# Kernel tuning notes

Measured on AMD Instinct MI355X. Metric: run time of the kernel, lower is better.

## Reference

```python
import jax, jax.numpy as jnp
import numpy as np

STRIDE = 16
BASE_SIZE = 16
RATIOS = (0.5, 1.0, 2.0)
SCALES = (8, 16, 32)
N_PRE_NMS = 3000
N_POST_NMS = 300
NMS_THRESH = 0.5
MIN_SIZE = 16.0


def _make_anchors(H, W):
    # base anchors centered at 0, [x1,y1,x2,y2]; ratio-major, scale-minor
    ba = []
    for r in RATIOS:
        for s in SCALES:
            w = BASE_SIZE * s * np.sqrt(1.0 / r)
            h = BASE_SIZE * s * np.sqrt(r)
            ba.append([-0.5 * w, -0.5 * h, 0.5 * w, 0.5 * h])
    ba = np.asarray(ba, np.float32)  # (9,4)
    xs = np.arange(W, dtype=np.float32) * STRIDE
    ys = np.arange(H, dtype=np.float32) * STRIDE
    X, Y = np.meshgrid(xs, ys)  # (H,W), h-major matches NHWC flatten order
    shifts = np.stack([X.ravel(), Y.ravel(), X.ravel(), Y.ravel()], 1)  # (H*W,4)
    return jnp.asarray((shifts[:, None, :] + ba[None, :, :]).reshape(-1, 4))


def _conv(x, w, b, pad):
    y = jax.lax.conv_general_dilated(x, w, (1, 1), [(pad, pad), (pad, pad)],
                                     dimension_numbers=('NCHW', 'OIHW', 'NCHW'))
    return y + b[None, :, None, None]


def _nms_keep(boxes, valid, thresh):
    # greedy NMS on score-sorted boxes; classic +1 area convention
    x1, y1, x2, y2 = boxes[:, 0], boxes[:, 1], boxes[:, 2], boxes[:, 3]
    areas = (x2 - x1 + 1.0) * (y2 - y1 + 1.0)
    n = boxes.shape[0]
    idx = jnp.arange(n)

    def body(i, keep):
        xx1 = jnp.maximum(x1[i], x1)
        yy1 = jnp.maximum(y1[i], y1)
        xx2 = jnp.minimum(x2[i], x2)
        yy2 = jnp.minimum(y2[i], y2)
        inter = jnp.clip(xx2 - xx1 + 1.0, 0.0) * jnp.clip(yy2 - yy1 + 1.0, 0.0)
        iou = inter / (areas[i] + areas - inter)
        sup = jnp.any((idx < i) & keep & (iou > thresh))
        return keep.at[i].set(keep[i] & (~sup))

    return jax.lax.fori_loop(0, n, body, valid)


def _rpn_forward(x, w_base, b_base, w_cls, b_cls, w_reg, b_reg):
    B, _, H, W = x.shape  # B == 1
    base = jax.nn.relu(_conv(x, w_base, b_base, 1))           # (1,512,H,W)
    locs = _conv(base, w_reg, b_reg, 0).transpose(0, 2, 3, 1).reshape(-1, 4)  # (H*W*9,4)
    cls = _conv(base, w_cls, b_cls, 0).transpose(0, 2, 3, 1).reshape(1, -1, 2)
    fg = jax.nn.softmax(cls, axis=-1)[0, :, 1]                # (H*W*9,)

    anchors = _make_anchors(H, W)
    aw = anchors[:, 2] - anchors[:, 0]
    ah = anchors[:, 3] - anchors[:, 1]
    acx = anchors[:, 0] + 0.5 * aw
    acy = anchors[:, 1] + 0.5 * ah
    cx = locs[:, 0] * aw + acx
    cy = locs[:, 1] * ah + acy
    w = jnp.exp(locs[:, 2]) * aw
    h = jnp.exp(locs[:, 3]) * ah
    boxes = jnp.stack([cx - 0.5 * w, cy - 0.5 * h, cx + 0.5 * w, cy + 0.5 * h], 1)

    img_w = float(W * STRIDE)
    img_h = float(H * STRIDE)
    boxes = jnp.stack([jnp.clip(boxes[:, 0], 0.0, img_w),
                       jnp.clip(boxes[:, 1], 0.0, img_h),
                       jnp.clip(boxes[:, 2], 0.0, img_w),
                       jnp.clip(boxes[:, 3], 0.0, img_h)], 1)
    valid = ((boxes[:, 2] - boxes[:, 0]) >= MIN_SIZE) & ((boxes[:, 3] - boxes[:, 1]) >= MIN_SIZE)

    masked = jnp.where(valid, fg, -jnp.inf)
    top_scores, top_idx = jax.lax.top_k(masked, N_PRE_NMS)   # descending, == argsort top-k
    bsel = boxes[top_idx]
    vsel = valid[top_idx]

    keep = _nms_keep(bsel, vsel, NMS_THRESH)
    rank = jnp.cumsum(keep.astype(jnp.int32)) - 1
    pos = jnp.where(keep & (rank < N_POST_NMS), rank, N_POST_NMS)  # out-of-range -> dropped
    rois = jnp.zeros((N_POST_NMS, 4), bsel.dtype).at[pos].set(bsel, mode='drop')
    # original scores[:n_post] over dim0 of shape (1,n_pre) is a no-op -> full (1,3000)
    return rois, top_scores[None, :]


def setup_inputs() -> dict:
    key = jax.random.key(0)
    ks = jax.random.split(key, 7)
    H = W = 128
    return {
        'x': jax.random.normal(ks[0], (1, 1024, H, W), jnp.float32),
        'w_base': jax.random.normal(ks[1], (512, 1024, 3, 3), jnp.float32) * 0.01,
        'b_base': jax.random.normal(ks[2], (512,), jnp.float32) * 0.01,
        'w_cls': jax.random.normal(ks[3], (18, 512, 1, 1), jnp.float32) * 0.01,
        'b_cls': jax.random.normal(ks[4], (18,), jnp.float32) * 0.01,
        'w_reg': jax.random.normal(ks[5], (36, 512, 1, 1), jnp.float32) * 0.01,
        'b_reg': jax.random.normal(ks[6], (36,), jnp.float32) * 0.01,
    }


def reference(x, w_base, b_base, w_cls, b_cls, w_reg, b_reg):
    return _rpn_forward(x, w_base, b_base, w_cls, b_cls, w_reg, b_reg)
```

## Files before the change

### kernel.cpp

```cpp
#include <hip/hip_runtime.h>
#include <cmath>

typedef unsigned long long u64;
typedef __attribute__((ext_vector_type(8))) short short8;
typedef __attribute__((ext_vector_type(4))) float f32x4;
typedef __attribute__((ext_vector_type(4))) double f64x4;

#define N_ANCH   147456
#define N_SCREEN 3600
#define N_PRE    3000
#define N_POST   300
#define NWORDS   47
#define SEL_CAP  4096

__device__ inline short f2bf(float f) {
    unsigned u = __float_as_uint(f);
    unsigned r = u + 0x7FFFu + ((u >> 16) & 1u);
    return (short)(r >> 16);
}

__global__ __launch_bounds__(256) void rpn_prep_xT(const float* __restrict__ x,
                                                   short* __restrict__ xT) {
    __shared__ short tile[32][258];
    const int h  = blockIdx.x;
    const int w0 = blockIdx.y * 32;
    const int c0 = blockIdx.z * 256;
    const int tid = threadIdx.x;
    const int wi = tid & 31, cs = tid >> 5;
    #pragma unroll
    for (int it = 0; it < 32; ++it) {
        int c = it * 8 + cs;
        float v = x[(size_t)(c0 + c) * 16384 + h * 128 + w0 + wi];
        tile[wi][c] = f2bf(v);
    }
    __syncthreads();
    #pragma unroll
    for (int it = 0; it < 32; ++it) {
        int i = tid + it * 256;
        int wj = i >> 8, c = i & 255;
        xT[((size_t)h * 128 + w0 + wj) * 1024 + c0 + c] = tile[wj][c];
    }
}

__global__ __launch_bounds__(256) void rpn_prep_wbf(const float* __restrict__ wb,
                                                    short* __restrict__ wT) {
    __shared__ float wtile[2304];
    const int oc = blockIdx.x;
    const int c0 = blockIdx.y * 256;
    const int tid = threadIdx.x;
    #pragma unroll
    for (int it = 0; it < 9; ++it) {
        int i = tid + it * 256;
        wtile[i] = wb[(size_t)oc * 9216 + c0 * 9 + i];
    }
    __syncthreads();
    #pragma unroll
    for (int it = 0; it < 9; ++it) {
        int i = tid + it * 256;
        int t = i >> 8, c = i & 255;
        wT[((size_t)t * 512 + oc) * 1024 + c0 + c] = f2bf(wtile[c * 9 + t]);
    }
}

__global__ __launch_bounds__(256) void rpn_prep_w(const float* __restrict__ wb,
                                                  float* __restrict__ wt) {
    __shared__ float tile[64][65];
    const int bx = blockIdx.x;
    const int by = blockIdx.y;
    const int tid = threadIdx.x;
    #pragma unroll
    for (int it = 0; it < 16; ++it) {
        int i = tid + it * 256;
        int r = i >> 6, c = i & 63;
        tile[r][c] = wb[(size_t)(by * 64 + r) * 9216 + bx * 64 + c];
    }
    __syncthreads();
    #pragma unroll
    for (int it = 0; it < 16; ++it) {
        int i = tid + it * 256;
        int r = i >> 6, c = i & 63;
        wt[(size_t)(bx * 64 + r) * 512 + by * 64 + c] = tile[c][r];
    }
}

__global__ void rpn_prep_wht(const float* __restrict__ wc, const float* __restrict__ wr,
                             float* __restrict__ wht) {
    int i = blockIdx.x * 256 + threadIdx.x;
    if (i >= 512 * 56) return;
    int c = i / 56, k = i - c * 56;
    float v = 0.f;
    if (k < 18)       v = wc[k * 512 + c];
    else if (k < 54)  v = wr[(k - 18) * 512 + c];
    wht[i] = v;
}

#define STAGE_LOADM(WREG, XREG, CN)                                            \
    {                                                                          \
        _Pragma("unroll")                                                      \
        for (int it = 0; it < 9; ++it)                                         \
            WREG[it] = *(const short8*)&wT[wgo[it] + (CN)];                    \
        _Pragma("unroll")                                                      \
        for (int it = 0; it < 4; ++it)                                         \
            XREG[it] = (xgo[it] >= 0) ? *(const short8*)&xT[xgo[it] + (CN)]    \
                                      : zer;                                   \
    }
#define STAGE_WRITEM(WREG, XREG)                                               \
    {                                                                          \
        _Pragma("unroll")                                                      \
        for (int it = 0; it < 9; ++it) *(short8*)&wsm[wlo[it]] = WREG[it];     \
        _Pragma("unroll")                                                      \
        for (int it = 0; it < 4; ++it)                                         \
            if (xlo[it] >= 0) *(short8*)&xsm[xlo[it]] = XREG[it];              \
    }
#define MFMA_CHUNKM()                                                          \
    {                                                                          \
        _Pragma("unroll")                                                      \
        for (int t = 0; t < 9; ++t) {                                          \
            int kh = t / 3, kw = t - kh * 3;                                   \
            int ra0 = t * 128 + wocB + l15;                                    \
            int ra1 = ra0 + 16;                                                \
            short8 a0 = *(const short8*)&wsm[ra0 * 32 + ((lg ^ ((ra0 >> 1) & 3)) << 3)]; \
            short8 a1 = *(const short8*)&wsm[ra1 * 32 + ((lg ^ ((ra1 >> 1) & 3)) << 3)]; \
            _Pragma("unroll")                                                  \
            for (int nf = 0; nf < 4; ++nf) {                                   \
                int rb = kh * 130 + wpx + nf * 16 + l15 + kw;                  \
                short8 b = *(const short8*)&xsm[rb * 32 + ((lg ^ ((rb >> 1) & 3)) << 3)]; \
                acc[0][nf] = __builtin_amdgcn_mfma_f32_16x16x32_bf16(a0, b, acc[0][nf], 0, 0, 0); \
                acc[1][nf] = __builtin_amdgcn_mfma_f32_16x16x32_bf16(a1, b, acc[1][nf], 0, 0, 0); \
            }                                                                  \
        }                                                                      \
    }

__global__ __launch_bounds__(512, 2) void rpn_screen_mfma(
    const short* __restrict__ xT, const short* __restrict__ wT,
    const float* __restrict__ bb, const float* __restrict__ wht_,
    float* __restrict__ logits) {
    const int row = blockIdx.x;
    const int ocB = blockIdx.y * 128;
    const int tid = threadIdx.x;
    const int wave = tid >> 6, lane = tid & 63;
    const int l15 = lane & 15, lg = lane >> 4;
    const int wocB = (wave & 3) * 32;
    const int wpx  = (wave >> 2) * 64;
    __shared__ __attribute__((aligned(16))) short wsm[1152 * 32];
    __shared__ __attribute__((aligned(16))) short xsm[390 * 32];

    size_t wgo[9];  int wlo[9];
    #pragma unroll
    for (int it = 0; it < 9; ++it) {
        int i = tid + it * 512;
        int r = i >> 2, s = i & 3;
        int t = r >> 7, ocl = r & 127;
        wgo[it] = ((size_t)t * 512 + ocB + ocl) * 1024 + s * 8;
        wlo[it] = r * 32 + ((s ^ ((r >> 1) & 3)) << 3);
    }
    long xgo[4]; int xlo[4];
    #pragma unroll
    for (int it = 0; it < 4; ++it) {
        int i = tid + it * 512;
        xlo[it] = -1; xgo[it] = -1;
        if (i < 1560) {
            int r = i >> 2, s = i & 3;
            int r3 = r / 130, col = r - r3 * 130;
            int h = row - 1 + r3, wc = col - 1;
            xlo[it] = r * 32 + ((s ^ ((r >> 1) & 3)) << 3);
            xgo[it] = (h >= 0 && h < 128 && wc >= 0 && wc < 128)
                      ? (long)(((size_t)h * 128 + wc) * 1024 + s * 8) : -1;
        }
    }

    f32x4 acc[2][4];
    #pragma unroll
    for (int mi = 0; mi < 2; ++mi)
        #pragma unroll
        for (int nf = 0; nf < 4; ++nf)
            acc[mi][nf] = (f32x4){0.f, 0.f, 0.f, 0.f};

    short8 wregA[9], xregA[4], wregB[9], xregB[4];
    const short8 zer = {0, 0, 0, 0, 0, 0, 0, 0};

    STAGE_LOADM(wregA, xregA, 0);
    STAGE_LOADM(wregB, xregB, 32);

    for (int i2 = 0; i2 < 16; ++i2) {
        int cA = i2 * 64;
        __syncthreads();
        STAGE_WRITEM(wregA, xregA);
        __syncthreads();
        if (cA + 64 < 1024) STAGE_LOADM(wregA, xregA, cA + 64);
        MFMA_CHUNKM();
        __syncthreads();
        STAGE_WRITEM(wregB, xregB);
        __syncthreads();
        if (cA + 96 < 1024) STAGE_LOADM(wregB, xregB, cA + 96);
        MFMA_CHUNKM();
    }

    float r_[8][4];
    #pragma unroll
    for (int mi = 0; mi < 2; ++mi)
        #pragma unroll
        for (int rr = 0; rr < 4; ++rr) {
            int ocg = ocB + wocB + mi * 16 + lg * 4 + rr;
            float bv = bb[ocg];
            #pragma unroll
            for (int nf = 0; nf < 4; ++nf)
                r_[mi * 4 + rr][nf] = fmaxf(acc[mi][nf][rr] + bv, 0.f);
        }
    float* lred = (float*)wsm;
    const int pxc = tid >> 2, qqc = tid & 3;
    for (int qc = 0; qc < 14; ++qc) {
        float wq[8][4];
        #pragma unroll
        for (int p = 0; p < 8; ++p) {
            int ocg = ocB + wocB + (p >> 2) * 16 + lg * 4 + (p & 3);
            float4 wv = *(const float4*)&wht_[(size_t)ocg * 56 + qc * 4];
            wq[p][0] = wv.x; wq[p][1] = wv.y; wq[p][2] = wv.z; wq[p][3] = wv.w;
        }
        __syncthreads();
        #pragma unroll
        for (int nf = 0; nf < 4; ++nf) {
            #pragma unroll
            for (int qq = 0; qq < 4; ++qq) {
                float s = 0.f;
                #pragma unroll
                for (int p = 0; p < 8; ++p) s = fmaf(r_[p][nf], wq[p][qq], s);
                s += __shfl_xor(s, 16);
                s += __shfl_xor(s, 32);
                if (lg == 0)
                    lred[(((wave & 3) * 128) + wpx + nf * 16 + l15) * 4 + qq] = s;
            }
        }
        __syncthreads();
        float v = lred[(0 * 128 + pxc) * 4 + qqc] + lred[(1 * 128 + pxc) * 4 + qqc]
                + lred[(2 * 128 + pxc) * 4 + qqc] + lred[(3 * 128 + pxc) * 4 + qqc];
        atomicAdd(&logits[(size_t)(row * 128 + pxc) * 56 + qc * 4 + qqc], v);
    }
}

__global__ void rpn_screen_decode(
    const float* __restrict__ logits, const float* __restrict__ bc,
    const float* __restrict__ br, unsigned* __restrict__ keys32,
    unsigned* __restrict__ hist1) {
    int aidx = blockIdx.x * 256 + threadIdx.x;
    if (aidx >= N_ANCH) return;
    int px = aidx / 9, a = aidx - px * 9;
    int wix = px & 127, hix = px >> 7;
    float Xf = (float)(wix * 16), Yf = (float)(hix * 16);
    int ri = a / 3, si = a - ri * 3;
    double rr  = (ri == 0) ? 0.5 : ((ri == 1) ? 1.0 : 2.0);
    double scl = (si == 0) ? 8.0 : ((si == 1) ? 16.0 : 32.0);
    double wA = 16.0 * scl * sqrt(1.0 / rr);
    double hA = 16.0 * scl * sqrt(rr);
    float c0 = (float)(-0.5 * wA), c1 = (float)(-0.5 * hA);
    float c2 = (float)( 0.5 * wA), c3 = (float)( 0.5 * hA);
    float ax1 = Xf + c0, ay1 = Yf + c1, ax2 = Xf + c2, ay2 = Yf + c3;
    float aw = ax2 - ax1, ah = ay2 - ay1;
    float acx = ax1 + 0.5f * aw, acy = ay1 + 0.5f * ah;
    const float* L = &logits[(size_t)px * 56];
    float l0 = L[2 * a]     + bc[2 * a];
    float l1 = L[2 * a + 1] + bc[2 * a + 1];
    float dx = L[18 + 4 * a + 0] + br[4 * a + 0];
    float dy = L[18 + 4 * a + 1] + br[4 * a + 1];
    float dw = L[18 + 4 * a + 2] + br[4 * a + 2];
    float dh = L[18 + 4 * a + 3] + br[4 * a + 3];
    float cx = dx * aw + acx, cy = dy * ah + acy;
    float bw = expf(dw) * aw, bh = expf(dh) * ah;
    float x1 = fminf(fmaxf(cx - 0.5f * bw, 0.f), 2048.f);
    float y1 = fminf(fmaxf(cy - 0.5f * bh, 0.f), 2048.f);
    float x2 = fminf(fmaxf(cx + 0.5f * bw, 0.f), 2048.f);
    float y2 = fminf(fmaxf(cy + 0.5f * bh, 0.f), 2048.f);
    bool valid = (x2 - x1 >= 12.0f) && (y2 - y1 >= 12.0f);
    float m = fmaxf(l0, l1);
    float e0 = expf(l0 - m), e1 = expf(l1 - m);
    float fg = e1 / (e0 + e1);
    float msk = valid ? fg : -INFINITY;
    unsigned kb = __float_as_uint(msk);
    kb = (kb & 0x80000000u) ? ~kb : (kb | 0x80000000u);
    keys32[aidx] = kb;
    atomicAdd(&hist1[kb >> 16], 1u);
}

__global__ void rpn_select1(const unsigned* __restrict__ hist, unsigned* __restrict__ meta) {
    __shared__ unsigned seg[256];
    __shared__ unsigned suf[257];
    int t = threadIdx.x;
    unsigned s = 0;
    for (int j = 0; j < 256; ++j) s += hist[t * 256 + j];
    seg[t] = s;
    __syncthreads();
    if (t == 0) {
        unsigned run = 0; suf[256] = 0;
        for (int q = 255; q >= 0; --q) { run += seg[q]; suf[q] = run; }
    }
    __syncthreads();
    if (suf[t + 1] < N_SCREEN && suf[t] >= N_SCREEN) {
        unsigned cum = suf[t + 1];
        for (int b = t * 256 + 255; b >= t * 256; --b) {
            unsigned prev = cum;
            cum += hist[b];
            if (cum >= N_SCREEN) { meta[0] = (unsigned)b; meta[1] = prev; break; }
        }
    }
}

__global__ void rpn_hist2(const unsigned* __restrict__ keys, const unsigned* __restrict__ meta,
                          unsigned* __restrict__ hist2) {
    int i = blockIdx.x * 256 + threadIdx.x;
    if (i >= N_ANCH) return;
    unsigned B = meta[0];
    unsigned k = keys[i];
    if ((k >> 16) == B) atomicAdd(&hist2[k & 0xFFFFu], 1u);
}

__global__ void rpn_select2(const unsigned* __restrict__ hist2, unsigned* __restrict__ meta) {
    __shared__ unsigned seg[256];
    __shared__ unsigned suf[257];
    int t = threadIdx.x;
    unsigned s = 0;
    for (int j = 0; j < 256; ++j) s += hist2[t * 256 + j];
    seg[t] = s;
    __syncthreads();
    if (t == 0) {
        unsigned run = 0; suf[256] = 0;
        for (int q = 255; q >= 0; --q) { run += seg[q]; suf[q] = run; }
    }
    __syncthreads();
    unsigned need = N_SCREEN - meta[1];
    if (suf[t + 1] < need && suf[t] >= need) {
        unsigned cum = suf[t + 1];
        for (int b = t * 256 + 255; b >= t * 256; --b) {
            cum += hist2[b];
            if (cum >= need) { meta[3] = (meta[0] << 16) | (unsigned)b; break; }
        }
    }
}

__global__ void rpn_compact(const unsigned* __restrict__ keys, unsigned* meta,
                            int* __restrict__ sel_idx, unsigned* __restrict__ pxflag) {
    int i = blockIdx.x * 256 + threadIdx.x;
    if (i >= N_ANCH) return;
    if (keys[i] >= meta[3]) {
        unsigned pos = atomicAdd(&meta[4], 1u);
        if (pos < SEL_CAP) {
            sel_idx[pos] = i;
            pxflag[i / 9] = 1u;
        }
    }
}

__global__ void rpn_px_compact(const unsigned* __restrict__ pxflag, unsigned* meta,
                               int* __restrict__ pxlist, int* __restrict__ pxslot) {
    int px = blockIdx.x * 256 + threadIdx.x;
    if (px >= 16384) return;
    if (pxflag[px]) {
        int slot = (int)atomicAdd(&meta[5], 1u);
        pxlist[slot] = px;
        pxslot[px] = slot;
    }
}

__global__ __launch_bounds__(256) void rpn_rescue_gemm(
    const float* __restrict__ x, const float* __restrict__ wt,
    const int* __restrict__ pxlist, const unsigned* __restrict__ meta,
    double* __restrict__ base64) {
    int npx = (int)meta[5];
    int s0 = blockIdx.x * 16;
    if (s0 >= npx) return;
    const int tid  = threadIdx.x;
    const int wave = tid >> 6, lane = tid & 63;
    const int l15 = lane & 15, lg = lane >> 4;
    const int ocg = blockIdx.y * 64 + wave * 16;
    __shared__ double xs[144][17];

    f64x4 p1 = (f64x4){0.0, 0.0, 0.0, 0.0};
    f64x4 p2 = (f64x4){0.0, 0.0, 0.0, 0.0};
    p1 = __builtin_amdgcn_mfma_f64_16x16x4f64((double)l15, 1.0, p1, 0, 0, 0);
    p2 = __builtin_amdgcn_mfma_f64_16x16x4f64(1.0, (double)l15, p2, 0, 0, 0);
    int srow[4], scol[4];
    #pragma unroll
    for (int r = 0; r < 4; ++r) {
        srow[r] = (int)(p1[r] * 0.25 + 0.5);
        scol[r] = (int)(p2[r] * 0.25 + 0.5);
    }

    int sp_off[9];
    int ch_of[9];
    #pragma unroll
    for (int it = 0; it < 9; ++it) {
        int j = tid + it * 256;
        int kk = j >> 4, slot = j & 15;
        int cl = kk / 9, tap = kk - cl * 9;
        int sg = s0 + slot;
        int pv = pxlist[(sg < npx) ? sg : s0];
        int yy = (pv >> 7) + tap / 3 - 1;
        int xx = (pv & 127) + tap % 3 - 1;
        sp_off[it] = (yy >= 0 && yy < 128 && xx >= 0 && xx < 128) ? (yy * 128 + xx) : -1;
        ch_of[it] = cl;
    }

    f64x4 acc = (f64x4){0.0, 0.0, 0.0, 0.0};
    float xreg[9];

    #pragma unroll
    for (int it = 0; it < 9; ++it)
        xreg[it] = (sp_off[it] >= 0) ? x[(size_t)ch_of[it] * 16384 + sp_off[it]] : 0.f;

    const size_t wlane = (size_t)(ocg + l15) + (size_t)lg * 512;
    for (int c0 = 0; c0 < 1024; c0 += 16) {
        __syncthreads();
        #pragma unroll
        for (int it = 0; it < 9; ++it) {
            int j = tid + it * 256;
            xs[j >> 4][j & 15] = (double)xreg[it];
        }
        __syncthreads();
        if (c0 + 16 < 1024) {
            #pragma unroll
            for (int it = 0; it < 9; ++it)
                xreg[it] = (sp_off[it] >= 0)
                           ? x[(size_t)(c0 + 16 + ch_of[it]) * 16384 + sp_off[it]] : 0.f;
        }
        const size_t wbase = (size_t)c0 * 4608 + wlane;
        #pragma unroll
        for (int ks = 0; ks < 36; ++ks) {
            double a = xs[ks * 4 + lg][l15];
            double b = (double)wt[wbase + (size_t)ks * 2048];
            acc = __builtin_amdgcn_mfma_f64_16x16x4f64(a, b, acc, 0, 0, 0);
        }
    }
    #pragma unroll
    for (int r = 0; r < 4; ++r) {
        int slot = s0 + srow[r];
        if (slot < npx)
            base64[(size_t)slot * 512 + ocg + scol[r]] = acc[r];
    }
}

__global__ __launch_bounds__(256) void rpn_rescue_heads(
    const double* __restrict__ base64, const float* __restrict__ wht,
    const float* __restrict__ bb, const float* __restrict__ bc,
    const float* __restrict__ br, const unsigned* __restrict__ meta,
    double* __restrict__ logits64) {
    int npx = (int)meta[5]; if (npx > SEL_CAP) npx = SEL_CAP;
    int slot0 = blockIdx.x * 4;
    if (slot0 >= npx) return;
    const int tid = threadIdx.x;
    __shared__ double bs[4][514];
    for (int i = tid; i < 4 * 512; i += 256) {
        int s = i >> 9, c = i & 511;
        int slt = slot0 + s;
        double v = (slt < npx) ? base64[(size_t)slt * 512 + c] : 0.0;
        double r = v + (double)bb[c];
        bs[s][c] = (r > 0.0) ? r : 0.0;
    }
    __syncthreads();
    if (tid < 224) {
        int s = tid / 56, q = tid - s * 56;
        int slt = slot0 + s;
        if (slt < npx) {
            double acc = (q < 18) ? (double)bc[q] : ((q < 54) ? (double)br[q - 18] : 0.0);
            const double* b = bs[s];
            #pragma unroll 8
            for (int c = 0; c < 512; ++c)
                acc = fma(b[c], (double)wht[c * 56 + q], acc);
            logits64[(size_t)slt * 56 + q] = acc;
        }
    }
}

__global__ void rpn_rescue_decode(
    const double* __restrict__ logits64, const int* __restrict__ sel_idx,
    const int* __restrict__ pxslot, const unsigned* __restrict__ meta,
    double* __restrict__ boxes_d, float* __restrict__ sc32, u64* __restrict__ sel) {
    int i = blockIdx.x * 256 + threadIdx.x;
    unsigned M = meta[4]; if (M > SEL_CAP) M = SEL_CAP;
    if (i >= (int)M) return;
    int aidx = sel_idx[i];
    int px = aidx / 9, a = aidx - px * 9;
    int slot = pxslot[px];
    int wix = px & 127, hix = px >> 7;
    float Xf = (float)(wix * 16), Yf = (float)(hix * 16);
    int ri = a / 3, si = a - ri * 3;
    double rr  = (ri == 0) ? 0.5 : ((ri == 1) ? 1.0 : 2.0);
    double scl = (si == 0) ? 8.0 : ((si == 1) ? 16.0 : 32.0);
    double wA = 16.0 * scl * sqrt(1.0 / rr);
    double hA = 16.0 * scl * sqrt(rr);
    float c0 = (float)(-0.5 * wA), c1 = (float)(-0.5 * hA);
    float c2 = (float)( 0.5 * wA), c3 = (float)( 0.5 * hA);
    float ax1 = Xf + c0, ay1 = Yf + c1, ax2 = Xf + c2, ay2 = Yf + c3;
    float awf = ax2 - ax1, ahf = ay2 - ay1;
    float acxf = ax1 + 0.5f * awf, acyf = ay1 + 0.5f * ahf;
    double aw = (double)awf, ah = (double)ahf;
    double acx = (double)acxf, acy = (double)acyf;
    const double* L = &logits64[(size_t)slot * 56];
    double l0 = L[2 * a], l1 = L[2 * a + 1];
    double dx = L[18 + 4 * a + 0], dy = L[18 + 4 * a + 1];
    double dw = L[18 + 4 * a + 2], dh = L[18 + 4 * a + 3];
    double cx = dx * aw + acx, cy = dy * ah + acy;
    double bw = exp(dw) * aw, bh = exp(dh) * ah;
    double x1 = fmin(fmax(cx - 0.5 * bw, 0.0), 2048.0);
    double y1 = fmin(fmax(cy - 0.5 * bh, 0.0), 2048.0);
    double x2 = fmin(fmax(cx + 0.5 * bw, 0.0), 2048.0);
    double y2 = fmin(fmax(cy + 0.5 * bh, 0.0), 2048.0);
    bool valid = (x2 - x1 >= 16.0) && (y2 - y1 >= 16.0);
    double m = fmax(l0, l1);
    double e0 = exp(l0 - m), e1 = exp(l1 - m);
    double fg = e1 / (e0 + e1);
    double msk = valid ? fg : -INFINITY;
    double* bd = &boxes_d[(size_t)aidx * 4];
    bd[0] = x1; bd[1] = y1; bd[2] = x2; bd[3] = y2;
    sc32[aidx] = (float)msk;
    long long ll = __double_as_longlong(msk);
    u64 u = (ll < 0) ? ~(u64)ll : ((u64)ll | 0x8000000000000000ull);
    sel[i] = (u & 0xFFFFFFFFFFFC0000ull) | (u64)(0x3FFFFu - (unsigned)aidx);
}

__global__ __launch_bounds__(1024) void rpn_sort(
    const u64* __restrict__ sel, const unsigned* __restrict__ meta,
    const double* __restrict__ boxes_d, const float* __restrict__ sc32,
    float* __restrict__ out, double* __restrict__ bsel, unsigned* __restrict__ vsel) {
    __shared__ u64 ss[SEL_CAP];
    int tid = threadIdx.x;
    int M = (int)meta[4]; if (M > SEL_CAP) M = SEL_CAP;
    for (int i = tid; i < SEL_CAP; i += 1024) ss[i] = (i < M) ? sel[i] : 0ULL;
    __syncthreads();
    for (int k = 2; k <= SEL_CAP; k <<= 1) {
        for (int j = k >> 1; j > 0; j >>= 1) {
            for (int i = tid; i < SEL_CAP; i += 1024) {
                int l = i ^ j;
                if (l > i) {
                    u64 a = ss[i], b = ss[l];
                    bool desc = (i & k) == 0;
                    if ((a < b) == desc) { ss[i] = b; ss[l] = a; }
                }
            }
            __syncthreads();
        }
    }
    for (int r = tid; r < N_PRE; r += 1024) {
        u64 key = ss[r];
        unsigned idx = 0x3FFFFu - (unsigned)(key & 0x3FFFFull);
        out[N_POST * 4 + r] = sc32[idx];
        const double* bd = &boxes_d[(size_t)idx * 4];
        double* dst = &bsel[(size_t)r * 4];
        dst[0] = bd[0]; dst[1] = bd[1]; dst[2] = bd[2]; dst[3] = bd[3];
        vsel[r] = (key >> 63) ? 1u : 0u;
    }
}

__global__ void rpn_nms_mask(const double* __restrict__ bsel, u64* __restrict__ mask) {
    int t = blockIdx.x * 256 + threadIdx.x;
    if (t >= N_PRE * NWORDS) return;
    int i = t / NWORDS, w = t - i * NWORDS;
    const double* bi = &bsel[(size_t)i * 4];
    double bix1 = bi[0], biy1 = bi[1], bix2 = bi[2], biy2 = bi[3];
    double ai = (bix2 - bix1 + 1.0) * (biy2 - biy1 + 1.0);
    u64 bits = 0ULL;
    int j0 = w * 64;
    for (int jj = 0; jj < 64; ++jj) {
        int j = j0 + jj;
        if (j >= N_PRE || j == i) continue;
        const double* bj = &bsel[(size_t)j * 4];
        double aj = (bj[2] - bj[0] + 1.0) * (bj[3] - bj[1] + 1.0);
        double xx1 = fmax(bix1, bj[0]), yy1 = fmax(biy1, bj[1]);
        double xx2 = fmin(bix2, bj[2]), yy2 = fmin(biy2, bj[3]);
        double iw = fmax(xx2 - xx1 + 1.0, 0.0), ih = fmax(yy2 - yy1 + 1.0, 0.0);
        double inter = iw * ih;
        double iou = inter / (ai + aj - inter);
        if (iou > 0.5) bits |= 1ULL << jj;
    }
    mask[(size_t)i * NWORDS + w] = bits;
}

__global__ __launch_bounds__(64) void rpn_nms_scan(
    const u64* __restrict__ mask, const unsigned* __restrict__ vsel,
    unsigned* __restrict__ keep, unsigned* __restrict__ rank) {
    int lane = threadIdx.x;
    u64 remv = 0ULL;
    int kc = 0;
    u64 pre[8];
    unsigned vpre[8];
    #pragma unroll
    for (int q = 0; q < 8; ++q) {
        pre[q]  = (lane < NWORDS) ? mask[(size_t)q * NWORDS + lane] : 0ULL;
        vpre[q] = vsel[q];
    }
    for (int i0 = 0; i0 < N_PRE; i0 += 8) {
        u64 nxt[8];
        unsigned vnxt[8];
        #pragma unroll
        for (int q = 0; q < 8; ++q) {
            int r = i0 + 8 + q;
            nxt[q]  = (r < N_PRE && lane < NWORDS) ? mask[(size_t)r * NWORDS + lane] : 0ULL;
            vnxt[q] = (r < N_PRE) ? vsel[r] : 0u;
        }
        #pragma unroll
        for (int q = 0; q < 8; ++q) {
            int i = i0 + q;
            int word = i >> 6, bit = i & 63;
            u64 rw = __shfl(remv, word);
            bool sup = (rw >> bit) & 1ULL;
            bool kp = (vpre[q] != 0u) && !sup;
            if (kp) remv |= pre[q];
            if (lane == 0) { keep[i] = kp ? 1u : 0u; rank[i] = (unsigned)kc; }
            kc += kp ? 1 : 0;
        }
        #pragma unroll
        for (int q = 0; q < 8; ++q) { pre[q] = nxt[q]; vpre[q] = vnxt[q]; }
    }
}

__global__ void rpn_finalize(const unsigned* __restrict__ keep, const unsigned* __restrict__ rank,
                             const double* __restrict__ bsel, float* __restrict__ out) {
    int i = blockIdx.x * 256 + threadIdx.x;
    if (i < N_PRE && keep[i] && rank[i] < N_POST) {
        const double* b = &bsel[(size_t)i * 4];
        float4 v = make_float4((float)b[0], (float)b[1], (float)b[2], (float)b[3]);
        ((float4*)out)[rank[i]] = v;
    }
}

extern "C" void kernel_launch(void* const* d_in, const int* in_sizes, int n_in,
                              void* d_out, int out_size, void* d_ws, size_t ws_size,
                              hipStream_t stream) {
    const float* x   = (const float*)d_in[0];
    const float* wb  = (const float*)d_in[1];
    const float* bb  = (const float*)d_in[2];
    const float* wc  = (const float*)d_in[3];
    const float* bc  = (const float*)d_in[4];
    const float* wr  = (const float*)d_in[5];
    const float* br  = (const float*)d_in[6];
    float* out = (float*)d_out;

    char* ws = (char*)d_ws;
    short*    xT       = (short*)(ws);
    float*    wt       = (float*)(ws);
    double*   base64   = (double*)(ws + 18874368);
    short*    wT       = (short*)(ws + 33554432);
    float*    logits32 = (float*)(ws + 42991616);
    float*    wht      = (float*)(ws + 46661632);
    double*   logits64 = (double*)(ws + 46776320);
    double*   boxes_d  = (double*)(ws + 48611328);
    float*    sc32     = (float*)(ws + 53329920);
    unsigned* keys32   = (unsigned*)(ws + 53919744);
    unsigned* hist1    = (unsigned*)(ws + 54509568);
    unsigned* hist2    = (unsigned*)(ws + 54771712);
    unsigned* meta     = (unsigned*)(ws + 55033856);
    int*      sel_idx  = (int*)(ws + 55034112);
    u64*      sel      = (u64*)(ws + 55050496);
    unsigned* pxflag   = (unsigned*)(ws + 55083264);
    int*      pxlist   = (int*)(ws + 55148800);
    int*      pxslot   = (int*)(ws + 55165184);
    double*   bsel     = (double*)(ws + 55230720);
    unsigned* vsel     = (unsigned*)(ws + 55326720);
    u64*      mask     = (u64*)(ws + 55338752);
    unsigned* keep     = (unsigned*)(ws + 56466752);
    unsigned* rank     = (unsigned*)(ws + 56478752);

    hipMemsetAsync(logits32, 0, 3670016, stream);
    hipMemsetAsync(hist1, 0, 262144 * 2 + 256, stream);
    hipMemsetAsync(pxflag, 0, 65536, stream);
    hipMemsetAsync(d_out, 0, N_POST * 4 * sizeof(float), stream);

    rpn_prep_xT      <<<dim3(128, 4, 4), 256, 0, stream>>>(x, xT);
    rpn_prep_wbf     <<<dim3(512, 4), 256, 0, stream>>>(wb, wT);
    rpn_prep_wht     <<<112, 256, 0, stream>>>(wc, wr, wht);
    rpn_screen_mfma  <<<dim3(128, 4), 512, 0, stream>>>(xT, wT, bb, wht, logits32);
    rpn_prep_w       <<<dim3(144, 8), 256, 0, stream>>>(wb, wt);
    rpn_screen_decode<<<576, 256, 0, stream>>>(logits32, bc, br, keys32, hist1);
    rpn_select1      <<<1, 256, 0, stream>>>(hist1, meta);
    rpn_hist2        <<<576, 256, 0, stream>>>(keys32, meta, hist2);
    rpn_select2      <<<1, 256, 0, stream>>>(hist2, meta);
    rpn_compact      <<<576, 256, 0, stream>>>(keys32, meta, sel_idx, pxflag);
    rpn_px_compact   <<<64, 256, 0, stream>>>(pxflag, meta, pxlist, pxslot);
    rpn_rescue_gemm  <<<dim3(256, 8), 256, 0, stream>>>(x, wt, pxlist, meta, base64);
    rpn_rescue_heads <<<1024, 256, 0, stream>>>(base64, wht, bb, bc, br, meta, logits64);
    rpn_rescue_decode<<<16, 256, 0, stream>>>(logits64, sel_idx, pxslot, meta,
                                              boxes_d, sc32, sel);
    rpn_sort         <<<1, 1024, 0, stream>>>(sel, meta, boxes_d, sc32, out, bsel, vsel);
    rpn_nms_mask     <<<(N_PRE * NWORDS + 255) / 256, 256, 0, stream>>>(bsel, mask);
    rpn_nms_scan     <<<1, 64, 0, stream>>>(mask, vsel, keep, rank);
    rpn_finalize     <<<12, 256, 0, stream>>>(keep, rank, bsel, out);
}
```

Baseline: 1.822 ms.

## Widen rescue GEMM tile to 64 pixels per block to reuse weights

The fp64 rescue GEMM now handles 64 candidate pixels per block instead of 16, keeping four MFMA accumulators per wave so that each weight value loaded from global memory feeds four MFMAs. This cuts redundant weight traffic and the number of blocks, but raises register pressure (36 prefetch registers plus 36 offsets) and shrinks the grid from 256x8 to 64x8, which may reduce occupancy when there are few candidate pixels.

Result: no change. 1.847 ms (+1.4%).

```diff
diff --git a/kernel.cpp b/kernel.cpp
--- a/kernel.cpp
+++ b/kernel.cpp
@@ -365,13 +365,13 @@
     const int* __restrict__ pxlist, const unsigned* __restrict__ meta,
     double* __restrict__ base64) {
     int npx = (int)meta[5];
-    int s0 = blockIdx.x * 16;
+    int s0 = blockIdx.x * 64;
     if (s0 >= npx) return;
     const int tid  = threadIdx.x;
     const int wave = tid >> 6, lane = tid & 63;
     const int l15 = lane & 15, lg = lane >> 4;
     const int ocg = blockIdx.y * 64 + wave * 16;
-    __shared__ double xs[144][17];
+    __shared__ double xs[144 * 66];
 
     f64x4 p1 = (f64x4){0.0, 0.0, 0.0, 0.0};
     f64x4 p2 = (f64x4){0.0, 0.0, 0.0, 0.0};
@@ -384,56 +384,65 @@
         scol[r] = (int)(p2[r] * 0.25 + 0.5);
     }
 
-    int sp_off[9];
-    int ch_of[9];
-    #pragma unroll
-    for (int it = 0; it < 9; ++it) {
-        int j = tid + it * 256;
-        int kk = j >> 4, slot = j & 15;
-        int cl = kk / 9, tap = kk - cl * 9;
-        int sg = s0 + slot;
-        int pv = pxlist[(sg < npx) ? sg : s0];
-        int yy = (pv >> 7) + tap / 3 - 1;
-        int xx = (pv & 127) + tap % 3 - 1;
-        sp_off[it] = (yy >= 0 && yy < 128 && xx >= 0 && xx < 128) ? (yy * 128 + xx) : -1;
-        ch_of[it] = cl;
-    }
-
-    f64x4 acc = (f64x4){0.0, 0.0, 0.0, 0.0};
-    float xreg[9];
-
-    #pragma unroll
-    for (int it = 0; it < 9; ++it)
-        xreg[it] = (sp_off[it] >= 0) ? x[(size_t)ch_of[it] * 16384 + sp_off[it]] : 0.f;
+    const int slot = tid & 63;
+    const int kkb  = tid >> 6;
+    int xoff[36];
+    {
+        int sg2 = s0 + slot;
+        int pv = pxlist[(sg2 < npx) ? sg2 : s0];
+        int py = pv >> 7, pxx = pv & 127;
+        #pragma unroll
+        for (int it = 0; it < 36; ++it) {
+            int kk = it * 4 + kkb;
+            int cl = kk / 9, tap = kk - cl * 9;
+            int yy = py + tap / 3 - 1;
+            int xx = pxx + tap % 3 - 1;
+            xoff[it] = (yy >= 0 && yy < 128 && xx >= 0 && xx < 128)
+                       ? (cl * 16384 + yy * 128 + xx) : -1;
+        }
+    }
+
+    f64x4 acc[4];
+    #pragma unroll
+    for (int s = 0; s < 4; ++s) acc[s] = (f64x4){0.0, 0.0, 0.0, 0.0};
+
+    float xreg[36];
+    #pragma unroll
+    for (int it = 0; it < 36; ++it)
+        xreg[it] = (xoff[it] >= 0) ? x[xoff[it]] : 0.f;
 
     const size_t wlane = (size_t)(ocg + l15) + (size_t)lg * 512;
     for (int c0 = 0; c0 < 1024; c0 += 16) {
         __syncthreads();
         #pragma unroll
-        for (int it = 0; it < 9; ++it) {
-            int j = tid + it * 256;
-            xs[j >> 4][j & 15] = (double)xreg[it];
-        }
+        for (int it = 0; it < 36; ++it)
+            xs[(it * 4 + kkb) * 66 + slot] = (double)xreg[it];
         __syncthreads();
         if (c0 + 16 < 1024) {
+            const size_t xb = (size_t)(c0 + 16) * 16384;
             #pragma unroll
-            for (int it = 0; it < 9; ++it)
-                xreg[it] = (sp_off[it] >= 0)
-                           ? x[(size_t)(c0 + 16 + ch_of[it]) * 16384 + sp_off[it]] : 0.f;
+            for (int it = 0; it < 36; ++it)
+                xreg[it] = (xoff[it] >= 0) ? x[xb + xoff[it]] : 0.f;
         }
         const size_t wbase = (size_t)c0 * 4608 + wlane;
         #pragma unroll
         for (int ks = 0; ks < 36; ++ks) {
-            double a = xs[ks * 4 + lg][l15];
             double b = (double)wt[wbase + (size_t)ks * 2048];
-            acc = __builtin_amdgcn_mfma_f64_16x16x4f64(a, b, acc, 0, 0, 0);
-        }
-    }
-    #pragma unroll
-    for (int r = 0; r < 4; ++r) {
-        int slot = s0 + srow[r];
-        if (slot < npx)
-            base64[(size_t)slot * 512 + ocg + scol[r]] = acc[r];
+            const double* ar = &xs[(ks * 4 + lg) * 66 + l15];
+            acc[0] = __builtin_amdgcn_mfma_f64_16x16x4f64(ar[0],  b, acc[0], 0, 0, 0);
+            acc[1] = __builtin_amdgcn_mfma_f64_16x16x4f64(ar[16], b, acc[1], 0, 0, 0);
+            acc[2] = __builtin_amdgcn_mfma_f64_16x16x4f64(ar[32], b, acc[2], 0, 0, 0);
+            acc[3] = __builtin_amdgcn_mfma_f64_16x16x4f64(ar[48], b, acc[3], 0, 0, 0);
+        }
+    }
+    #pragma unroll
+    for (int sg2 = 0; sg2 < 4; ++sg2) {
+        #pragma unroll
+        for (int r = 0; r < 4; ++r) {
+            int slt = s0 + sg2 * 16 + srow[r];
+            if (slt < npx)
+                base64[(size_t)slt * 512 + ocg + scol[r]] = acc[sg2][r];
+        }
     }
 }
 
@@ -674,7 +683,7 @@
     rpn_select2      <<<1, 256, 0, stream>>>(hist2, meta);
     rpn_compact      <<<576, 256, 0, stream>>>(keys32, meta, sel_idx, pxflag);
     rpn_px_compact   <<<64, 256, 0, stream>>>(pxflag, meta, pxlist, pxslot);
-    rpn_rescue_gemm  <<<dim3(256, 8), 256, 0, stream>>>(x, wt, pxlist, meta, base64);
+    rpn_rescue_gemm  <<<dim3(64, 8), 256, 0, stream>>>(x, wt, pxlist, meta, base64);
     rpn_rescue_heads <<<1024, 256, 0, stream>>>(base64, wht, bb, bc, br, meta, logits64);
     rpn_rescue_decode<<<16, 256, 0, stream>>>(logits64, sel_idx, pxslot, meta,
                                               boxes_d, sc32, sel);
```
